# Optimization experiments

Hardware: AMD Instinct MI355X
Metric: run time of the kernel (lower is better)

## Reference

```python
import jax, jax.numpy as jnp
import numpy as np

HIDDEN_DIM = 512
SCALE = float(np.sqrt(HIDDEN_DIM))  # hidden_dim ** 0.5, matches torch


def setup_inputs() -> dict:
    key = jax.random.key(0)
    ks = jax.random.split(key, 4)
    B, S, D_IN = 8, 4096, 64
    x = jax.random.normal(ks[0], (B, S, D_IN), dtype=jnp.float32)
    # Linear weights stored as [in, out] (transposed vs torch's [out, in])
    Wq = jax.random.normal(ks[1], (D_IN, HIDDEN_DIM), dtype=jnp.float32) * (1.0 / np.sqrt(D_IN))
    Wk = jax.random.normal(ks[2], (D_IN, HIDDEN_DIM), dtype=jnp.float32) * (1.0 / np.sqrt(D_IN))
    Wv = jax.random.normal(ks[3], (D_IN, HIDDEN_DIM), dtype=jnp.float32) * (1.0 / np.sqrt(D_IN))
    bq = jnp.zeros((HIDDEN_DIM,), dtype=jnp.float32)
    bk = jnp.zeros((HIDDEN_DIM,), dtype=jnp.float32)
    bv = jnp.zeros((HIDDEN_DIM,), dtype=jnp.float32)
    return {"x": x, "Wq": Wq, "bq": bq, "Wk": Wk, "bk": bk, "Wv": Wv, "bv": bv}


def reference(x, Wq, bq, Wk, bk, Wv, bv):
    # Q/K/V projections: [B, S, H]
    Q = jnp.einsum('bsd,dh->bsh', x, Wq) + bq
    K = jnp.einsum('bsd,dh->bsh', x, Wk) + bk
    V = jnp.einsum('bsd,dh->bsh', x, Wv) + bv
    # Naive single-head attention with full [B, S, S] score matrix,
    # matching the original torch math exactly.
    scores = jnp.einsum('bqh,bkh->bqk', Q, K) / SCALE
    attn = jax.nn.softmax(scores, axis=-1)
    return jnp.einsum('bqk,bkh->bqh', attn, V)
```

## Files before the change

kernel.cpp:

```cpp
#include <hip/hip_runtime.h>
#include <hip/hip_bf16.h>
#include <math.h>


#define SS 4096
#define DD 64
#define HH 512

#define CSCALE ((float)(1.4426950408889634 * 0.04419417382415922))

typedef __bf16 bf16x8 __attribute__((ext_vector_type(8)));
typedef float  f32x4  __attribute__((ext_vector_type(4)));
typedef float  f32x16 __attribute__((ext_vector_type(16)));
typedef unsigned int u32x4 __attribute__((ext_vector_type(4)));

__device__ __forceinline__ float b2f(__hip_bfloat16 v) { return __bfloat162float(v); }

__device__ __forceinline__ f32x4 mfma16(bf16x8 a, bf16x8 b, f32x4 c) {
  return __builtin_amdgcn_mfma_f32_16x16x32_bf16(a, b, c, 0, 0, 0);
}
__device__ __forceinline__ f32x16 mfma32(bf16x8 a, bf16x8 b, f32x16 c) {
  return __builtin_amdgcn_mfma_f32_32x32x16_bf16(a, b, c, 0, 0, 0);
}

__device__ __forceinline__ unsigned pack2(float a, float b) {
  float2 f2; f2.x = a; f2.y = b;
  __hip_bfloat162 h2 = __float22bfloat162_rn(f2);
  unsigned u; __builtin_memcpy(&u, &h2, 4);
  return u;
}

__device__ __forceinline__ float loadf(const void* p, size_t i, int isF32) {
  return isF32 ? ((const float*)p)[i] : b2f(((const __hip_bfloat16*)p)[i]);
}
__device__ __forceinline__ void load8f(const void* p, size_t i, int isF32, float* o) {
  if (isF32) {
    const float4 a = *(const float4*)((const float*)p + i);
    const float4 b = *(const float4*)((const float*)p + i + 4);
    o[0]=a.x; o[1]=a.y; o[2]=a.z; o[3]=a.w; o[4]=b.x; o[5]=b.y; o[6]=b.z; o[7]=b.w;
  } else {
    const bf16x8 v = *(const bf16x8*)((const __hip_bfloat16*)p + i);
#pragma unroll
    for (int k = 0; k < 8; ++k) { __hip_bfloat16 h; __builtin_memcpy(&h, ((const unsigned short*)&v) + k, 2); o[k] = b2f(h); }
  }
}

__device__ __forceinline__ int probe_f32(const void* Wq, int lane) {
  const unsigned short* h = (const unsigned short*)Wq;
  unsigned int bits = ((unsigned int)h[lane * 2]) << 16;
  float v; __builtin_memcpy(&v, &bits, 4);
  v = fabsf(v);
  if (!isfinite(v) || v > 1e10f) v = 1e10f;
  for (int off = 1; off < 64; off <<= 1) v = fmaxf(v, __shfl_xor(v, off, 64));
  return (v > 1e6f) ? 1 : 0;
}

__global__ __launch_bounds__(256) void prep_kernel(
    const void* __restrict__ Wq, const void* __restrict__ Wk,
    const void* __restrict__ Wv, const void* __restrict__ bq,
    const void* __restrict__ bk, __hip_bfloat16* __restrict__ MT,
    float* __restrict__ u, float* __restrict__ w_, float* __restrict__ c_,
    __hip_bfloat16* __restrict__ wvT, int* __restrict__ flag) {
  const int t = threadIdx.x, blk = blockIdx.x;
  __shared__ int fS;
  if (t < 64) { const int f = probe_f32(Wq, t); if (t == 0) fS = f; }
  __syncthreads();
  const int isF32 = fS;
  if (blk < 64) {
    __shared__ float red[256];
    const int i = blk, j = t >> 2, part = t & 3;
    float acc = 0.f, aq[8], ak[8];
    for (int c = 0; c < 16; ++c) {
      load8f(Wq, (size_t)i * HH + part * 128 + c * 8, isF32, aq);
      load8f(Wk, (size_t)j * HH + part * 128 + c * 8, isF32, ak);
#pragma unroll
      for (int k = 0; k < 8; ++k) acc = fmaf(aq[k], ak[k], acc);
    }
    red[t] = acc;
    __syncthreads();
    if (t < 64)
      MT[t * 64 + i] = __float2bfloat16(red[t*4] + red[t*4+1] + red[t*4+2] + red[t*4+3]);
  } else if (blk == 64) {
    __shared__ float pu[256], pw[256], pc[64];
    const int i = t & 63, part = t >> 6;
    float au = 0.f, aw = 0.f, v1[8], v2[8];
    for (int c = 0; c < 16; ++c) {
      load8f(Wq, (size_t)i * HH + part * 128 + c * 8, isF32, v1);
      load8f(bk, part * 128 + c * 8, isF32, v2);
#pragma unroll
      for (int k = 0; k < 8; ++k) au = fmaf(v1[k], v2[k], au);
      load8f(Wk, (size_t)i * HH + part * 128 + c * 8, isF32, v1);
      load8f(bq, part * 128 + c * 8, isF32, v2);
#pragma unroll
      for (int k = 0; k < 8; ++k) aw = fmaf(v1[k], v2[k], aw);
    }
    pu[t] = au; pw[t] = aw;
    if (t < 64) {
      float s = 0.f;
      for (int e = 0; e < 8; ++e)
        s = fmaf(loadf(bq, t * 8 + e, isF32), loadf(bk, t * 8 + e, isF32), s);
      pc[t] = s;
    }
    __syncthreads();
    if (t < 64) {
      u[t]  = pu[t] + pu[t+64] + pu[t+128] + pu[t+192];
      w_[t] = pw[t] + pw[t+64] + pw[t+128] + pw[t+192];
    }
    if (t == 0) {
      float s = 0.f;
      for (int e = 0; e < 64; ++e) s += pc[e];
      *c_ = s;
      *flag = isF32;
    }
  } else {
    const int base = (blk - 65) * 2048 + t;
    for (int r = 0; r < 8; ++r) {
      const int e = base + r * 256;
      const int h = e >> 6, d = e & 63;
      wvT[e] = __float2bfloat16(loadf(Wv, (size_t)d * HH + h, isF32));
    }
  }
}

__global__ __launch_bounds__(256) void proj_kernel(
    const void* __restrict__ xraw, const __hip_bfloat16* __restrict__ MT,
    const float* __restrict__ u, const float* __restrict__ w_,
    const float* __restrict__ c_, __hip_bfloat16* __restrict__ xc,
    __hip_bfloat16* __restrict__ y, float* __restrict__ qb,
    float* __restrict__ kb, __hip_bfloat16* __restrict__ xT,
    const int* __restrict__ flag) {
  __shared__ __hip_bfloat16 xs[64 * 72];
  __shared__ __hip_bfloat16 Ms[64 * 72];
  __shared__ __hip_bfloat16 st[64 * 72];
  __shared__ float us[64], wl[64];
  __shared__ float cs;

  const int t = threadIdx.x;
  const int isF32 = *flag;
  {
    const int r = t >> 2, cb = (t & 3) * 16;
    *(bf16x8*)(&Ms[r * 72 + cb])     = *(const bf16x8*)(MT + r * 64 + cb);
    *(bf16x8*)(&Ms[r * 72 + cb + 8]) = *(const bf16x8*)(MT + r * 64 + cb + 8);
  }
  if (t < 64) { us[t] = u[t]; wl[t] = w_[t]; }
  if (t == 0) cs = *c_;

  const int b = blockIdx.x & 7;
  const int sbase = (blockIdx.x >> 3) * 64;
  const int rbase = b * SS + sbase;

  for (int i = 0; i < 2; ++i) {
    const int e = i * 256 + t;
    const int row = e >> 3, col = (e & 7) * 8;
    float v[8];
    load8f(xraw, (size_t)(rbase + row) * DD + col, isF32, v);
    __hip_bfloat16* dp = xs + row * 72 + col;
#pragma unroll
    for (int k = 0; k < 8; ++k) dp[k] = __float2bfloat16(v[k]);
  }
  __syncthreads();

  const int wv = t >> 6, lane = t & 63;
  const int l16 = lane & 15, quad = lane >> 4;
  const bf16x8 A0 = *(const bf16x8*)(&xs[(wv * 16 + l16) * 72 + quad * 8]);
  const bf16x8 A1 = *(const bf16x8*)(&xs[(wv * 16 + l16) * 72 + 32 + quad * 8]);
  float yC[4][4];
#pragma unroll
  for (int nt = 0; nt < 4; ++nt) {
    const bf16x8 B0 = *(const bf16x8*)(&Ms[(nt * 16 + l16) * 72 + quad * 8]);
    const bf16x8 B1 = *(const bf16x8*)(&Ms[(nt * 16 + l16) * 72 + 32 + quad * 8]);
    f32x4 C = (f32x4){0.f, 0.f, 0.f, 0.f};
    C = mfma16(A0, B0, C);
    C = mfma16(A1, B1, C);
#pragma unroll
    for (int r = 0; r < 4; ++r) yC[nt][r] = C[r];
  }

  {
    const int q = t >> 2, pp = (t & 3) * 16;
    float qa = 0.f, ka = 0.f;
#pragma unroll
    for (int dd = 0; dd < 16; ++dd) {
      const int d = pp + dd;
      const float xv = b2f(xs[q * 72 + d]);
      qa = fmaf(xv, us[d], qa);
      ka = fmaf(xv, wl[d], ka);
    }
    qa += __shfl_xor(qa, 1, 64); qa += __shfl_xor(qa, 2, 64);
    ka += __shfl_xor(ka, 1, 64); ka += __shfl_xor(ka, 2, 64);
    if ((t & 3) == 0) {
      qb[rbase + q] = (qa + cs) * CSCALE;
      kb[rbase + q] = ka * CSCALE;
    }
  }

  for (int i = 0; i < 2; ++i) {
    const int e = i * 256 + t;
    const int row = e >> 3, col = (e & 7) * 8;
    *(bf16x8*)(xc + (size_t)(rbase + row) * DD + col) = *(const bf16x8*)(xs + row * 72 + col);
  }

#pragma unroll
  for (int nt = 0; nt < 4; ++nt)
#pragma unroll
    for (int r = 0; r < 4; ++r)
      st[(wv * 16 + quad * 4 + r) * 72 + nt * 16 + l16] = __float2bfloat16(yC[nt][r]);
  __syncthreads();
  {
    const int r = t >> 2, cb = (t & 3) * 16;
    *(bf16x8*)(y + (size_t)(rbase + r) * DD + cb)     = *(const bf16x8*)(&st[r * 72 + cb]);
    *(bf16x8*)(y + (size_t)(rbase + r) * DD + cb + 8) = *(const bf16x8*)(&st[r * 72 + cb + 8]);
  }
  __syncthreads();

  {
    const int d = t >> 2, sc = (t & 3) * 16;
#pragma unroll
    for (int k = 0; k < 16; ++k)
      st[d * 72 + sc + k] = xs[(sc + k) * 72 + d];
  }
  __syncthreads();
  {
    const int d = t >> 2, sc = (t & 3) * 16;
    __hip_bfloat16* xp = xT + ((size_t)b * DD + d) * SS + sbase + sc;
    *(bf16x8*)(xp)     = *(const bf16x8*)(&st[d * 72 + sc]);
    *(bf16x8*)(xp + 8) = *(const bf16x8*)(&st[d * 72 + sc + 8]);
  }
}

__global__ __launch_bounds__(256) void attn_split(
    const __hip_bfloat16* __restrict__ x,
    const __hip_bfloat16* __restrict__ y,
    const float* __restrict__ qb, const float* __restrict__ kb,
    const __hip_bfloat16* __restrict__ xT,
    float* __restrict__ Opart, float* __restrict__ lpart, int lgs) {
  __shared__ __hip_bfloat16 xs[2][32 * 72];
  __shared__ __hip_bfloat16 vsm[2][64 * 40];
  const int tid = threadIdx.x;
  const int wv = tid >> 6, lane = tid & 63;
  const int l32 = lane & 31, hi = lane >> 5;
  const int b = blockIdx.x & 7;
  const int nspl = 1 << lgs;
  const int ks = (blockIdx.x >> 3) & (nspl - 1);
  const int qg = blockIdx.x >> (3 + lgs);
  const int kspl = SS >> lgs;
  const int koff = ks * kspl;
  const size_t rowq = ((size_t)b << 12) + (size_t)qg * 128 + wv * 32;

  bf16x8 Y[4];
#pragma unroll
  for (int mi = 0; mi < 4; ++mi)
    Y[mi] = *(const bf16x8*)(y + (rowq + l32) * DD + mi * 16 + hi * 8);
  const float qbl = qb[rowq + l32];

  const int sxr = tid >> 3, sxc = (tid & 7) * 8;
  const int g = sxr >> 2;
  const int taur = (sxr & 3) + 4 * ((g & 4) | ((g & 1) << 1) | ((g >> 1) & 1));
  const int svd = tid >> 2, svc = (tid & 3) * 8;
  const __hip_bfloat16* gx = x + ((size_t)b * SS + koff + sxr) * DD + sxc;
  const __hip_bfloat16* gv = xT + ((size_t)b * DD + svd) * SS + koff + svc;
  const float* kbp = kb + (size_t)b * SS + koff + hi * 8;

  bf16x8 nx = *(const bf16x8*)gx;
  bf16x8 nv = *(const bf16x8*)gv;
  *(bf16x8*)(&xs[0][taur * 72 + sxc]) = nx;
  *(bf16x8*)(&vsm[0][svd * 40 + svc]) = nv;
  nx = *(const bf16x8*)(gx + 32 * DD);
  nv = *(const bf16x8*)(gv + 32);
  __syncthreads();

  f32x16 O0, O1;
#pragma unroll
  for (int r = 0; r < 16; ++r) { O0[r] = 0.f; O1[r] = 0.f; }
  float lp = 0.f;

  for (int kt = 0; kt < kspl; kt += 32) {
    const int p = (kt >> 5) & 1, np = p ^ 1;
    if (kt + 32 < kspl) {
      *(bf16x8*)(&xs[np][taur * 72 + sxc]) = nx;
      *(bf16x8*)(&vsm[np][svd * 40 + svc]) = nv;
      if (kt + 64 < kspl) {
        nx = *(const bf16x8*)(gx + (size_t)(kt + 64) * DD);
        nv = *(const bf16x8*)(gv + (kt + 64));
      }
    }
    const f32x4 kb0a = *(const f32x4*)(kbp + kt);
    const f32x4 kb0b = *(const f32x4*)(kbp + kt + 4);
    const f32x4 kb1a = *(const f32x4*)(kbp + kt + 16);
    const f32x4 kb1b = *(const f32x4*)(kbp + kt + 20);

    const bf16x8 A0 = *(const bf16x8*)(&xs[p][l32 * 72 + hi * 8]);
    const bf16x8 A1 = *(const bf16x8*)(&xs[p][l32 * 72 + 16 + hi * 8]);
    const bf16x8 A2 = *(const bf16x8*)(&xs[p][l32 * 72 + 32 + hi * 8]);
    const bf16x8 A3 = *(const bf16x8*)(&xs[p][l32 * 72 + 48 + hi * 8]);

    f32x16 S;
#pragma unroll
    for (int r = 0; r < 16; ++r) S[r] = 0.f;
    S = mfma32(A0, Y[0], S);
    S = mfma32(A1, Y[1], S);
    S = mfma32(A2, Y[2], S);
    S = mfma32(A3, Y[3], S);

    float pv[16];
#pragma unroll
    for (int r = 0; r < 16; ++r) {
      const float kv = (r < 4) ? kb0a[r & 3]
                     : (r < 8) ? kb0b[r & 3]
                     : (r < 12) ? kb1a[r & 3] : kb1b[r & 3];
      pv[r] = __builtin_amdgcn_exp2f(fmaf(S[r], CSCALE, qbl + kv));
    }
    {
      float s0 = (pv[0]+pv[1]) + (pv[2]+pv[3]);
      float s1 = (pv[4]+pv[5]) + (pv[6]+pv[7]);
      float s2 = (pv[8]+pv[9]) + (pv[10]+pv[11]);
      float s3 = (pv[12]+pv[13]) + (pv[14]+pv[15]);
      lp += (s0 + s1) + (s2 + s3);
    }
    u32x4 R0, R1;
    R0[0] = pack2(pv[0], pv[1]);  R0[1] = pack2(pv[2], pv[3]);
    R0[2] = pack2(pv[4], pv[5]);  R0[3] = pack2(pv[6], pv[7]);
    R1[0] = pack2(pv[8], pv[9]);  R1[1] = pack2(pv[10], pv[11]);
    R1[2] = pack2(pv[12], pv[13]); R1[3] = pack2(pv[14], pv[15]);
    bf16x8 Pf0, Pf1;
    __builtin_memcpy(&Pf0, &R0, 16);
    __builtin_memcpy(&Pf1, &R1, 16);

    const bf16x8 V00 = *(const bf16x8*)(&vsm[p][l32 * 40 + hi * 8]);
    const bf16x8 V10 = *(const bf16x8*)(&vsm[p][l32 * 40 + 16 + hi * 8]);
    const bf16x8 V01 = *(const bf16x8*)(&vsm[p][(l32 + 32) * 40 + hi * 8]);
    const bf16x8 V11 = *(const bf16x8*)(&vsm[p][(l32 + 32) * 40 + 16 + hi * 8]);

    O0 = mfma32(Pf0, V00, O0);
    O0 = mfma32(Pf1, V10, O0);
    O1 = mfma32(Pf0, V01, O1);
    O1 = mfma32(Pf1, V11, O1);

    __syncthreads();
  }

  lp += __shfl_xor(lp, 32, 64);
  const size_t NP = (size_t)SS * 8;
  if (hi == 0) lpart[(size_t)ks * NP + rowq + l32] = lp;

  float* Op = Opart + ((size_t)ks * NP + rowq) * 64;
#pragma unroll
  for (int r = 0; r < 16; ++r) {
    const int qrow = (r & 3) + 8 * (r >> 2) + 4 * hi;
    Op[(size_t)qrow * 64 + l32]      = O0[r];
    Op[(size_t)qrow * 64 + 32 + l32] = O1[r];
  }
}

__global__ __launch_bounds__(128) void combine_kernel(
    const float* __restrict__ Opart, const float* __restrict__ lpart,
    const __hip_bfloat16* __restrict__ wvT, const void* __restrict__ bv_raw,
    void* __restrict__ out_raw, const int* __restrict__ flag, int nspl) {
  const int tid = threadIdx.x;
  const int wv = tid >> 6, lane = tid & 63;
  const int l16 = lane & 15, quad = lane >> 4;
  const int bb = blockIdx.x & 7;
  const int gg = (blockIdx.x >> 3) & 127;
  const int hh = blockIdx.x >> 10;
  const size_t q0 = ((size_t)bb << 12) + (size_t)gg * 32 + (size_t)wv * 16;
  const int isF32 = *flag;
  const size_t NP = (size_t)SS * 8;

  float lsum = 0.f;
  for (int s = 0; s < nspl; ++s) lsum += lpart[(size_t)s * NP + q0 + l16];
  const float linv = (lsum > 0.f) ? 1.0f / lsum : 0.f;

  float vlo[8], vhi[8];
#pragma unroll
  for (int j = 0; j < 8; ++j) { vlo[j] = 0.f; vhi[j] = 0.f; }
  for (int s = 0; s < nspl; ++s) {
    const float* p0 = Opart + ((size_t)s * NP + q0 + l16) * 64 + quad * 8;
#pragma unroll
    for (int j = 0; j < 8; j += 4) {
      const float4 a = *(const float4*)(p0 + j);
      vlo[j]   += a.x; vlo[j+1] += a.y; vlo[j+2] += a.z; vlo[j+3] += a.w;
      const float4 c = *(const float4*)(p0 + 32 + j);
      vhi[j]   += c.x; vhi[j+1] += c.y; vhi[j+2] += c.z; vhi[j+3] += c.w;
    }
  }
  u32x4 Rlo, Rhi;
#pragma unroll
  for (int j = 0; j < 4; ++j) {
    Rlo[j] = pack2(vlo[2*j] * linv, vlo[2*j+1] * linv);
    Rhi[j] = pack2(vhi[2*j] * linv, vhi[2*j+1] * linv);
  }
  bf16x8 Alo, Ahi;
  __builtin_memcpy(&Alo, &Rlo, 16);
  __builtin_memcpy(&Ahi, &Rhi, 16);

  float* outf = (float*)out_raw;
  __hip_bfloat16* outb = (__hip_bfloat16*)out_raw;
  const int ht0 = hh * 16;
#pragma unroll 4
  for (int ht = ht0; ht < ht0 + 16; ++ht) {
    const __hip_bfloat16* wp = wvT + (size_t)(ht * 16 + l16) * DD + quad * 8;
    const bf16x8 Wlo = *(const bf16x8*)wp;
    const bf16x8 Whi = *(const bf16x8*)(wp + 32);
    f32x4 C = (f32x4){0.f, 0.f, 0.f, 0.f};
    C = mfma16(Alo, Wlo, C);
    C = mfma16(Ahi, Whi, C);
    const float bvv = loadf(bv_raw, ht * 16 + l16, isF32);
#pragma unroll
    for (int r = 0; r < 4; ++r) {
      const size_t oidx = (q0 + quad * 4 + r) * HH + ht * 16 + l16;
      const float val = C[r] + bvv;
      if (isF32) outf[oidx] = val;
      else       outb[oidx] = __float2bfloat16(val);
    }
  }
}

__global__ __launch_bounds__(256) void attn_kernel(
    const __hip_bfloat16* __restrict__ x,
    const __hip_bfloat16* __restrict__ y,
    const float* __restrict__ qb, const float* __restrict__ kb,
    const __hip_bfloat16* __restrict__ xT,
    const __hip_bfloat16* __restrict__ wvT,
    const void* __restrict__ bv_raw,
    void* __restrict__ out_raw, const int* __restrict__ flag) {
  __shared__ __hip_bfloat16 xs[2][32 * 72];
  __shared__ __hip_bfloat16 vsm[2][64 * 40];
  __shared__ float kbl[SS];
  const int tid = threadIdx.x;
  const int wv = tid >> 6, lane = tid & 63;
  const int l16 = lane & 15, quad = lane >> 4;
  const int b = blockIdx.x & 7;
  const int qt = (blockIdx.x >> 3) * 4 + wv;
  const size_t rowq = ((size_t)b << 12) + ((size_t)qt << 4);
  const int isF32 = *flag;

  const __hip_bfloat16* xb  = x  + ((size_t)b * SS) * DD;
  const __hip_bfloat16* xTb = xT + ((size_t)b * DD) * SS;
  const float* kbb = kb + ((size_t)b * SS);

  const __hip_bfloat16* yp = y + (rowq + l16) * DD + quad * 8;
  const bf16x8 Ylo = *(const bf16x8*)yp;
  const bf16x8 Yhi = *(const bf16x8*)(yp + 32);
  const float qbl = qb[rowq + l16];

  const int sxr = tid >> 3, sxc = (tid & 7) * 8;
  const int taur = (sxr & 3) + ((sxr >> 3) << 2) + (((sxr >> 2) & 1) << 4);
  const int svd = tid >> 2, svc = (tid & 3) * 8;
  const __hip_bfloat16* gx = xb + (size_t)sxr * DD + sxc;
  const __hip_bfloat16* gv = xTb + (size_t)svd * SS + svc;

#pragma unroll
  for (int j = 0; j < 4; ++j) {
    const int c = j * 256 + tid;
    *(f32x4*)(&kbl[c * 4]) = *(const f32x4*)(kbb + c * 4);
  }

  bf16x8 nx = *(const bf16x8*)gx;
  bf16x8 nv = *(const bf16x8*)gv;
  *(bf16x8*)(&xs[0][taur * 72 + sxc]) = nx;
  *(bf16x8*)(&vsm[0][svd * 40 + svc]) = nv;
  nx = *(const bf16x8*)(gx + 32 * DD);
  nv = *(const bf16x8*)(gv + 32);
  __syncthreads();

  bf16x8 onesb;
#pragma unroll
  for (int j = 0; j < 8; ++j) onesb[j] = (__bf16)1.0f;

  f32x4 O[4];
#pragma unroll
  for (int n = 0; n < 4; ++n) O[n] = (f32x4){0.f, 0.f, 0.f, 0.f};
  f32x4 Ol = (f32x4){0.f, 0.f, 0.f, 0.f};

  for (int kt = 0; kt < SS; kt += 32) {
    const int p = (kt >> 5) & 1, np = p ^ 1;
    if (kt + 32 < SS) {
      *(bf16x8*)(&xs[np][taur * 72 + sxc]) = nx;
      *(bf16x8*)(&vsm[np][svd * 40 + svc]) = nv;
      if (kt + 64 < SS) {
        nx = *(const bf16x8*)(gx + (size_t)(kt + 64) * DD);
        nv = *(const bf16x8*)(gv + (kt + 64));
      }
    }
    const bf16x8 B00 = *(const bf16x8*)(&xs[p][l16 * 72 + quad * 8]);
    const bf16x8 B01 = *(const bf16x8*)(&xs[p][l16 * 72 + 32 + quad * 8]);
    const bf16x8 B10 = *(const bf16x8*)(&xs[p][(16 + l16) * 72 + quad * 8]);
    const bf16x8 B11 = *(const bf16x8*)(&xs[p][(16 + l16) * 72 + 32 + quad * 8]);
    const bf16x8 V0 = *(const bf16x8*)(&vsm[p][l16 * 40 + quad * 8]);
    const bf16x8 V1 = *(const bf16x8*)(&vsm[p][(16 + l16) * 40 + quad * 8]);
    const bf16x8 V2 = *(const bf16x8*)(&vsm[p][(32 + l16) * 40 + quad * 8]);
    const bf16x8 V3 = *(const bf16x8*)(&vsm[p][(48 + l16) * 40 + quad * 8]);

    f32x4 S0 = (f32x4){0.f, 0.f, 0.f, 0.f};
    f32x4 S1 = (f32x4){0.f, 0.f, 0.f, 0.f};
    S0 = mfma16(B00, Ylo, S0);
    S0 = mfma16(B01, Yhi, S0);
    S1 = mfma16(B10, Ylo, S1);
    S1 = mfma16(B11, Yhi, S1);

    const f32x4 kb0 = *(const f32x4*)(&kbl[kt + quad * 8]);
    const f32x4 kb1 = *(const f32x4*)(&kbl[kt + quad * 8 + 4]);

    float p0[4], p1[4];
#pragma unroll
    for (int r = 0; r < 4; ++r) {
      p0[r] = __builtin_amdgcn_exp2f(fmaf(S0[r], CSCALE, qbl + kb0[r]));
      p1[r] = __builtin_amdgcn_exp2f(fmaf(S1[r], CSCALE, qbl + kb1[r]));
    }
    u32x4 R;
    R[0] = pack2(p0[0], p0[1]);
    R[1] = pack2(p0[2], p0[3]);
    R[2] = pack2(p1[0], p1[1]);
    R[3] = pack2(p1[2], p1[3]);
    bf16x8 Pf;
    __builtin_memcpy(&Pf, &R, 16);

    O[0] = mfma16(Pf, V0, O[0]);
    O[1] = mfma16(Pf, V1, O[1]);
    O[2] = mfma16(Pf, V2, O[2]);
    O[3] = mfma16(Pf, V3, O[3]);
    Ol = mfma16(Pf, onesb, Ol);

    __syncthreads();
  }

  float inv_l[4];
#pragma unroll
  for (int r = 0; r < 4; ++r)
    inv_l[r] = (Ol[r] > 0.f) ? 1.0f / Ol[r] : 0.f;
  __hip_bfloat16* pl = &xs[0][0] + wv * 1152;
#pragma unroll
  for (int n = 0; n < 4; ++n)
#pragma unroll
    for (int r = 0; r < 4; ++r) {
      const int row = quad * 4 + r;
      pl[row * 72 + n * 16 + l16] = __float2bfloat16(O[n][r] * inv_l[r]);
    }
  __syncthreads();
  const bf16x8 Alo = *(const bf16x8*)(pl + l16 * 72 + quad * 8);
  const bf16x8 Ahi = *(const bf16x8*)(pl + l16 * 72 + 32 + quad * 8);

  float* outf = (float*)out_raw;
  __hip_bfloat16* outb = (__hip_bfloat16*)out_raw;
#pragma unroll 4
  for (int ht = 0; ht < 32; ++ht) {
    const __hip_bfloat16* wp = wvT + (size_t)(ht * 16 + l16) * DD + quad * 8;
    const bf16x8 Wlo = *(const bf16x8*)wp;
    const bf16x8 Whi = *(const bf16x8*)(wp + 32);
    f32x4 C = (f32x4){0.f, 0.f, 0.f, 0.f};
    C = mfma16(Alo, Wlo, C);
    C = mfma16(Ahi, Whi, C);
    const float bvv = loadf(bv_raw, ht * 16 + l16, isF32);
#pragma unroll
    for (int r = 0; r < 4; ++r) {
      const size_t oidx = (rowq + quad * 4 + r) * HH + ht * 16 + l16;
      const float val = C[r] + bvv;
      if (isF32) outf[oidx] = val;
      else       outb[oidx] = __float2bfloat16(val);
    }
  }
}

extern "C" void kernel_launch(void* const* d_in, const int* in_sizes, int n_in,
                              void* d_out, int out_size, void* d_ws,
                              size_t ws_size, hipStream_t stream) {
  char* ws = (char*)d_ws;
  int*   flag = (int*)(ws + 0);
  __hip_bfloat16* MT = (__hip_bfloat16*)(ws + 1024);
  float* u    = (float*)(ws + 9216);
  float* w_   = (float*)(ws + 9728);
  float* c_   = (float*)(ws + 10240);
  __hip_bfloat16* wvT = (__hip_bfloat16*)(ws + 32768);
  __hip_bfloat16* xc  = (__hip_bfloat16*)(ws + 131072);
  __hip_bfloat16* y   = (__hip_bfloat16*)(ws + 4325376);
  float* qb = (float*)(ws + 8519680);
  float* kb = (float*)(ws + 8650752);
  __hip_bfloat16* xT = (__hip_bfloat16*)(ws + 8781824);
  float* Opart = (float*)(ws + 16777216);
  const size_t NP = (size_t)SS * 8;
  const size_t need4 = 16777216UL + 4UL * NP * 64 * 4 + 4UL * NP * 4;
  const size_t need2 = 16777216UL + 2UL * NP * 64 * 4 + 2UL * NP * 4;

  prep_kernel<<<81, 256, 0, stream>>>(d_in[1], d_in[3], d_in[5], d_in[2],
                                      d_in[4], MT, u, w_, c_, wvT, flag);
  proj_kernel<<<512, 256, 0, stream>>>(d_in[0], MT, u, w_, c_, xc, y, qb, kb,
                                       xT, flag);
  if (ws_size >= need4) {
    float* lpart = (float*)(ws + 16777216 + 4UL * NP * 64 * 4);
    attn_split<<<1024, 256, 0, stream>>>(xc, y, qb, kb, xT, Opart, lpart, 2);
    combine_kernel<<<2048, 128, 0, stream>>>(Opart, lpart, wvT, d_in[6], d_out,
                                             flag, 4);
  } else if (ws_size >= need2) {
    float* lpart = (float*)(ws + 16777216 + 2UL * NP * 64 * 4);
    attn_split<<<512, 256, 0, stream>>>(xc, y, qb, kb, xT, Opart, lpart, 1);
    combine_kernel<<<2048, 128, 0, stream>>>(Opart, lpart, wvT, d_in[6], d_out,
                                             flag, 2);
  } else {
    attn_kernel<<<512, 256, 0, stream>>>(xc, y, qb, kb, xT, wvT, d_in[6],
                                         d_out, flag);
  }
}
```

Before: 190.6 us.

## Compute softmax row sums via MFMA and restructure combine to stage via LDS

The attention split kernel drops the per-row qb bias from the exponent, since it cancels in softmax normalization. It now computes the row sum of probabilities with an extra MFMA against a ones vector instead of scalar adds and a cross-lane shuffle. The combine kernel now runs one 256-thread block per 32 queries and reduces each partial only once into LDS, where four waves share the normalized tile. Previously several blocks per query group each re-read the partial outputs. The risk is that the extra MFMA adds matrix-pipe work, and the row sum now comes from bf16-rounded probabilities.

```diff
diff --git a/kernel.cpp b/kernel.cpp
--- a/kernel.cpp
+++ b/kernel.cpp
@@ -251,7 +251,6 @@
 #pragma unroll
   for (int mi = 0; mi < 4; ++mi)
     Y[mi] = *(const bf16x8*)(y + (rowq + l32) * DD + mi * 16 + hi * 8);
-  const float qbl = qb[rowq + l32];
 
   const int sxr = tid >> 3, sxc = (tid & 7) * 8;
   const int g = sxr >> 2;
@@ -269,10 +268,13 @@
   nv = *(const bf16x8*)(gv + 32);
   __syncthreads();
 
-  f32x16 O0, O1;
-#pragma unroll
-  for (int r = 0; r < 16; ++r) { O0[r] = 0.f; O1[r] = 0.f; }
-  float lp = 0.f;
+  bf16x8 onesb;
+#pragma unroll
+  for (int j = 0; j < 8; ++j) onesb[j] = (__bf16)1.0f;
+
+  f32x16 O0, O1, Ol;
+#pragma unroll
+  for (int r = 0; r < 16; ++r) { O0[r] = 0.f; O1[r] = 0.f; Ol[r] = 0.f; }
 
   for (int kt = 0; kt < kspl; kt += 32) {
     const int p = (kt >> 5) & 1, np = p ^ 1;
@@ -308,14 +310,7 @@
       const float kv = (r < 4) ? kb0a[r & 3]
                      : (r < 8) ? kb0b[r & 3]
                      : (r < 12) ? kb1a[r & 3] : kb1b[r & 3];
-      pv[r] = __builtin_amdgcn_exp2f(fmaf(S[r], CSCALE, qbl + kv));
-    }
-    {
-      float s0 = (pv[0]+pv[1]) + (pv[2]+pv[3]);
-      float s1 = (pv[4]+pv[5]) + (pv[6]+pv[7]);
-      float s2 = (pv[8]+pv[9]) + (pv[10]+pv[11]);
-      float s3 = (pv[12]+pv[13]) + (pv[14]+pv[15]);
-      lp += (s0 + s1) + (s2 + s3);
+      pv[r] = __builtin_amdgcn_exp2f(fmaf(S[r], CSCALE, kv));
     }
     u32x4 R0, R1;
     R0[0] = pack2(pv[0], pv[1]);  R0[1] = pack2(pv[2], pv[3]);
@@ -335,13 +330,18 @@
     O0 = mfma32(Pf1, V10, O0);
     O1 = mfma32(Pf0, V01, O1);
     O1 = mfma32(Pf1, V11, O1);
+    Ol = mfma32(Pf0, onesb, Ol);
+    Ol = mfma32(Pf1, onesb, Ol);
 
     __syncthreads();
   }
 
-  lp += __shfl_xor(lp, 32, 64);
   const size_t NP = (size_t)SS * 8;
-  if (hi == 0) lpart[(size_t)ks * NP + rowq + l32] = lp;
+  if (l32 == 0) {
+#pragma unroll
+    for (int r = 0; r < 16; ++r)
+      lpart[(size_t)ks * NP + rowq + (r & 3) + 8 * (r >> 2) + 4 * hi] = Ol[r];
+  }
 
   float* Op = Opart + ((size_t)ks * NP + rowq) * 64;
 #pragma unroll
@@ -352,46 +352,52 @@
   }
 }
 
-__global__ __launch_bounds__(128) void combine_kernel(
+__global__ __launch_bounds__(256) void combine_kernel(
     const float* __restrict__ Opart, const float* __restrict__ lpart,
     const __hip_bfloat16* __restrict__ wvT, const void* __restrict__ bv_raw,
     void* __restrict__ out_raw, const int* __restrict__ flag, int nspl) {
+  __shared__ __hip_bfloat16 pa[32 * 72];
+  __shared__ float lsI[32];
   const int tid = threadIdx.x;
+  const int bb = blockIdx.x & 7;
+  const int gg = blockIdx.x >> 3;
+  const size_t q0 = ((size_t)bb << 12) + (size_t)gg * 32;
+  const int isF32 = *flag;
+  const size_t NP = (size_t)SS * 8;
+
+  if (tid < 32) {
+    float ls = 0.f;
+    for (int s = 0; s < nspl; ++s) ls += lpart[(size_t)s * NP + q0 + tid];
+    lsI[tid] = (ls > 0.f) ? 1.0f / ls : 0.f;
+  }
+  const int mq = tid >> 3, md = (tid & 7) * 8;
+  float acc[8];
+#pragma unroll
+  for (int j = 0; j < 8; ++j) acc[j] = 0.f;
+  for (int s = 0; s < nspl; ++s) {
+    const float* pp = Opart + ((size_t)s * NP + q0 + mq) * 64 + md;
+    const float4 a = *(const float4*)pp;
+    const float4 c = *(const float4*)(pp + 4);
+    acc[0] += a.x; acc[1] += a.y; acc[2] += a.z; acc[3] += a.w;
+    acc[4] += c.x; acc[5] += c.y; acc[6] += c.z; acc[7] += c.w;
+  }
+  __syncthreads();
+  {
+    const float linv = lsI[mq];
+    u32x4 R;
+#pragma unroll
+    for (int j = 0; j < 4; ++j)
+      R[j] = pack2(acc[2*j] * linv, acc[2*j+1] * linv);
+    __builtin_memcpy(&pa[mq * 72 + md], &R, 16);
+  }
+  __syncthreads();
+
   const int wv = tid >> 6, lane = tid & 63;
   const int l16 = lane & 15, quad = lane >> 4;
-  const int bb = blockIdx.x & 7;
-  const int gg = (blockIdx.x >> 3) & 127;
-  const int hh = blockIdx.x >> 10;
-  const size_t q0 = ((size_t)bb << 12) + (size_t)gg * 32 + (size_t)wv * 16;
-  const int isF32 = *flag;
-  const size_t NP = (size_t)SS * 8;
-
-  float lsum = 0.f;
-  for (int s = 0; s < nspl; ++s) lsum += lpart[(size_t)s * NP + q0 + l16];
-  const float linv = (lsum > 0.f) ? 1.0f / lsum : 0.f;
-
-  float vlo[8], vhi[8];
-#pragma unroll
-  for (int j = 0; j < 8; ++j) { vlo[j] = 0.f; vhi[j] = 0.f; }
-  for (int s = 0; s < nspl; ++s) {
-    const float* p0 = Opart + ((size_t)s * NP + q0 + l16) * 64 + quad * 8;
-#pragma unroll
-    for (int j = 0; j < 8; j += 4) {
-      const float4 a = *(const float4*)(p0 + j);
-      vlo[j]   += a.x; vlo[j+1] += a.y; vlo[j+2] += a.z; vlo[j+3] += a.w;
-      const float4 c = *(const float4*)(p0 + 32 + j);
-      vhi[j]   += c.x; vhi[j+1] += c.y; vhi[j+2] += c.z; vhi[j+3] += c.w;
-    }
-  }
-  u32x4 Rlo, Rhi;
-#pragma unroll
-  for (int j = 0; j < 4; ++j) {
-    Rlo[j] = pack2(vlo[2*j] * linv, vlo[2*j+1] * linv);
-    Rhi[j] = pack2(vhi[2*j] * linv, vhi[2*j+1] * linv);
-  }
-  bf16x8 Alo, Ahi;
-  __builtin_memcpy(&Alo, &Rlo, 16);
-  __builtin_memcpy(&Ahi, &Rhi, 16);
+  const int qh = wv & 1, hh = wv >> 1;
+  const __hip_bfloat16* par = &pa[(qh * 16 + l16) * 72];
+  const bf16x8 Alo = *(const bf16x8*)(par + quad * 8);
+  const bf16x8 Ahi = *(const bf16x8*)(par + 32 + quad * 8);
 
   float* outf = (float*)out_raw;
   __hip_bfloat16* outb = (__hip_bfloat16*)out_raw;
@@ -407,7 +413,7 @@
     const float bvv = loadf(bv_raw, ht * 16 + l16, isF32);
 #pragma unroll
     for (int r = 0; r < 4; ++r) {
-      const size_t oidx = (q0 + quad * 4 + r) * HH + ht * 16 + l16;
+      const size_t oidx = (q0 + qh * 16 + quad * 4 + r) * HH + ht * 16 + l16;
       const float val = C[r] + bvv;
       if (isF32) outf[oidx] = val;
       else       outb[oidx] = __float2bfloat16(val);
@@ -588,12 +594,12 @@
   if (ws_size >= need4) {
     float* lpart = (float*)(ws + 16777216 + 4UL * NP * 64 * 4);
     attn_split<<<1024, 256, 0, stream>>>(xc, y, qb, kb, xT, Opart, lpart, 2);
-    combine_kernel<<<2048, 128, 0, stream>>>(Opart, lpart, wvT, d_in[6], d_out,
+    combine_kernel<<<1024, 256, 0, stream>>>(Opart, lpart, wvT, d_in[6], d_out,
                                              flag, 4);
   } else if (ws_size >= need2) {
     float* lpart = (float*)(ws + 16777216 + 2UL * NP * 64 * 4);
     attn_split<<<512, 256, 0, stream>>>(xc, y, qb, kb, xT, Opart, lpart, 1);
-    combine_kernel<<<2048, 128, 0, stream>>>(Opart, lpart, wvT, d_in[6], d_out,
+    combine_kernel<<<1024, 256, 0, stream>>>(Opart, lpart, wvT, d_in[6], d_out,
                                              flag, 2);
   } else {
     attn_kernel<<<512, 256, 0, stream>>>(xc, y, qb, kb, xT, wvT, d_in[6],
```

Result: faster. 183.9 us (-3.5%).
